# Kernel optimization log

Hardware: AMD Instinct MI355X
Metric: run time of the kernel (lower is better)

## Reference

```python
import jax, jax.numpy as jnp
import numpy as np

EPS = 1.1920929e-07  # torch RMSNorm default eps = finfo(float32).eps

def rmsnorm(x, w):
    return x * jax.lax.rsqrt(jnp.mean(x * x, axis=-1, keepdims=True) + EPS) * w

def setup_inputs() -> dict:
    key = jax.random.key(0)
    ks = jax.random.split(key, 12)
    D, H, SC, ST = 1024, 16, 64, 16
    B, T = 2, 2048
    s = 0.02
    return {
        "x": jax.random.normal(ks[0], (B, T, D), jnp.float32),
        "qkv_w": jax.random.normal(ks[1], (3 * D, D), jnp.float32) * s,
        "o_w": jax.random.normal(ks[2], (D, D), jnp.float32) * s,
        "norm1_w": jnp.ones((D,), jnp.float32),
        "norm2_w": jnp.ones((D,), jnp.float32),
        "in_w": jax.random.normal(ks[3], (SC, D), jnp.float32) * s,
        "out_w": jax.random.normal(ks[4], (D, SC), jnp.float32) * s,  # zeros in torch init; randn for nontrivial baseline
        "A_log": jax.random.normal(ks[5], (SC, ST), jnp.float32) * 0.1,
        "Bp_w": jax.random.normal(ks[6], (ST, SC), jnp.float32) * s,
        "Cp_w": jax.random.normal(ks[7], (ST, SC), jnp.float32) * s,
        "dt_w": jax.random.normal(ks[8], (SC, SC), jnp.float32) * s,
        "dt_b": jnp.full((SC,), -3.0, jnp.float32),
        "gate_w": jax.random.normal(ks[9], (SC, D), jnp.float32) * s,
    }

def selective_scan(h, in_w, out_w, A_log, Bp_w, Cp_w, dt_w, dt_b, gate_w):
    B, T, D = h.shape
    SC, ST = A_log.shape
    z = h @ in_w.T                      # [B,T,SC]
    gate = jax.nn.silu(h @ gate_w.T)    # [B,T,SC]
    A = -jnp.exp(A_log)                 # [SC,ST]
    Bi = z @ Bp_w.T                     # [B,T,ST]
    Ci = z @ Cp_w.T                     # [B,T,ST]
    dt = jax.nn.softplus(z @ dt_w.T + dt_b)  # [B,T,SC]
    A_bar = 1.0 + dt[..., None] * A     # [B,T,SC,ST]

    def step(state, inp):
        a_bar, dtz_t, b_t, c_t = inp    # [B,SC,ST],[B,SC],[B,ST],[B,ST]
        state = a_bar * state + dtz_t[:, :, None] * b_t[:, None, :]
        y = jnp.sum(state * c_t[:, None, :], axis=-1)  # [B,SC]
        return state, y

    init = jnp.zeros((B, SC, ST), h.dtype)
    xs = (jnp.swapaxes(A_bar, 0, 1), jnp.swapaxes(dt * z, 0, 1),
          jnp.swapaxes(Bi, 0, 1), jnp.swapaxes(Ci, 0, 1))
    _, ys = jax.lax.scan(step, init, xs)      # [T,B,SC]
    y = jnp.swapaxes(ys, 0, 1) * gate         # [B,T,SC]
    return y @ out_w.T                        # [B,T,D]

def reference(x, qkv_w, o_w, norm1_w, norm2_w, in_w, out_w, A_log, Bp_w, Cp_w, dt_w, dt_b, gate_w):
    B, T, D = x.shape
    H = 16
    hd = D // H
    h = rmsnorm(x, norm1_w)
    qkv = (h @ qkv_w.T).reshape(B, T, 3, H, hd)
    qkv = jnp.transpose(qkv, (2, 0, 3, 1, 4))  # [3,B,H,T,hd]
    q, k, v = qkv[0], qkv[1], qkv[2]
    attn = jnp.einsum('bhqd,bhkd->bhqk', q, k) / np.sqrt(hd).astype(np.float32)
    mask = jnp.tril(jnp.ones((T, T), bool))
    attn = jnp.where(mask, attn, -jnp.inf)
    attn = jax.nn.softmax(attn, axis=-1)
    out = jnp.einsum('bhqk,bhkd->bhqd', attn, v)
    out = jnp.transpose(out, (0, 2, 1, 3)).reshape(B, T, D)
    x = x + out @ o_w.T
    h2 = rmsnorm(x, norm2_w)
    x = x + selective_scan(h2, in_w, out_w, A_log, Bp_w, Cp_w, dt_w, dt_b, gate_w)
    return x
```

## Files before the change

kernel.cpp:

```cpp
#include <hip/hip_runtime.h>
#include <hip/hip_bf16.h>
#include <math.h>

typedef __hip_bfloat16 bf16;
typedef __attribute__((ext_vector_type(4))) float v_f32x4;
typedef __attribute__((ext_vector_type(4))) unsigned short v_u16x4;
typedef __attribute__((ext_vector_type(8))) unsigned short v_u16x8;
typedef __attribute__((ext_vector_type(8))) __bf16 v_bf16x8;
typedef __attribute__((ext_vector_type(4))) __bf16 v_bf16x4;
typedef __attribute__((ext_vector_type(4))) short v_s16x4;

#define NB 2
#define NT 2048
#define ND 1024
#define NH 16
#define NSC 64
#define NST 16
#define NM (NB*NT)
#define RMS_EPS 1.1920929e-07f
#define NCHUNK 32
#define CLEN 64

__device__ inline float b2f(unsigned short u) {
  union { unsigned int i; float f; } v; v.i = ((unsigned int)u) << 16; return v.f;
}
__device__ inline unsigned short f2b(float f) {
  union { float f; unsigned int i; } v; v.f = f;
  unsigned int r = (v.i + 0x7FFF + ((v.i >> 16) & 1)) >> 16;
  return (unsigned short)r;
}

__device__ inline v_f32x4 mfma16(v_bf16x4 a, v_bf16x4 b, v_f32x4 c) {
#if __has_builtin(__builtin_amdgcn_mfma_f32_16x16x16_bf16)
  return __builtin_amdgcn_mfma_f32_16x16x16_bf16(a, b, c, 0, 0, 0);
#else
  union U { v_bf16x4 h; v_s16x4 s; };
  U ua, ub; ua.h = a; ub.h = b;
  return __builtin_amdgcn_mfma_f32_16x16x16bf16_1k(ua.s, ub.s, c, 0, 0, 0);
#endif
}

__device__ inline void gl_lds16(const bf16* g, bf16* l) {
  __builtin_amdgcn_global_load_lds((__attribute__((address_space(1))) void*)g,
                                   (__attribute__((address_space(3))) void*)l,
                                   16, 0, 0);
}

__global__ __launch_bounds__(256) void cvt_rms_kernel(
    const float* __restrict__ qkv_w, const float* __restrict__ o_w,
    const float* __restrict__ out_w, const float* __restrict__ in_w,
    const float* __restrict__ gate_w, const float* __restrict__ dt_w,
    const float* __restrict__ Bp_w, const float* __restrict__ Cp_w,
    bf16* __restrict__ qkvw_b, bf16* __restrict__ ow_b, bf16* __restrict__ outw_b,
    bf16* __restrict__ W1, bf16* __restrict__ W2,
    const float* __restrict__ x, const float* __restrict__ n1w, bf16* __restrict__ h) {
  const int blk = blockIdx.x, t = threadIdx.x;
  if (blk >= 4295) {
    const int row = blk - 4295;
    v_f32x4 xv = *(const v_f32x4*)(x + (size_t)row * ND + t * 4);
    float s = xv[0]*xv[0] + xv[1]*xv[1] + xv[2]*xv[2] + xv[3]*xv[3];
    #pragma unroll
    for (int off = 32; off; off >>= 1) s += __shfl_xor(s, off, 64);
    __shared__ float red[4];
    __shared__ float scale_s;
    if ((t & 63) == 0) red[t >> 6] = s;
    __syncthreads();
    if (t == 0) scale_s = rsqrtf((red[0] + red[1] + red[2] + red[3]) * (1.0f / ND) + RMS_EPS);
    __syncthreads();
    float sc = scale_s;
    v_f32x4 wv = *(const v_f32x4*)(n1w + t * 4);
    v_u16x4 o;
    o[0] = f2b(xv[0] * sc * wv[0]);
    o[1] = f2b(xv[1] * sc * wv[1]);
    o[2] = f2b(xv[2] * sc * wv[2]);
    o[3] = f2b(xv[3] * sc * wv[3]);
    *(v_u16x4*)((unsigned short*)h + (size_t)row * ND + t * 4) = o;
    return;
  }
  const float* src; bf16* dst; int base;
  if (blk < 3072)      { src = qkv_w;  dst = qkvw_b;      base = blk; }
  else if (blk < 4096) { src = o_w;    dst = ow_b;        base = blk - 3072; }
  else if (blk < 4160) { src = out_w;  dst = outw_b;      base = blk - 4096; }
  else if (blk < 4224) { src = in_w;   dst = W1;          base = blk - 4160; }
  else if (blk < 4288) { src = gate_w; dst = W1 + 65536;  base = blk - 4224; }
  else if (blk < 4292) { src = dt_w;   dst = W2;          base = blk - 4288; }
  else if (blk == 4292){ src = Bp_w;   dst = W2 + 4096;   base = 0; }
  else if (blk == 4293){ src = Cp_w;   dst = W2 + 5120;   base = 0; }
  else {
    v_u16x8 z;
    #pragma unroll
    for (int i = 0; i < 8; i++) z[i] = 0;
    *(v_u16x8*)(W2 + 6144 + t * 8) = z;
    return;
  }
  int i = base * 256 + t;
  v_f32x4 v = ((const v_f32x4*)src)[i];
  v_u16x4 o;
  o[0] = f2b(v[0]); o[1] = f2b(v[1]); o[2] = f2b(v[2]); o[3] = f2b(v[3]);
  ((v_u16x4*)dst)[i] = o;
}

template <bool RES, bool OUTF32>
__global__ __launch_bounds__(256) void gemm_bt_kernel(
    const bf16* __restrict__ A, const bf16* __restrict__ Bw,
    const float* __restrict__ res, void* __restrict__ Cout, int N, int K, int lda) {
  __shared__ alignas(16) bf16 As[128 * 32];
  __shared__ alignas(16) bf16 Bs[128 * 32];
  const int tid = threadIdx.x;
  const int wid = tid >> 6;
  const int lane = tid & 63;
  const int c = lane & 15;
  const int quad = lane >> 4;
  const int m0 = blockIdx.y * 128;
  const int n0 = blockIdx.x * 128;
  const int wm = (wid >> 1) * 64;
  const int wn = (wid & 1) * 64;
  const int srow = tid >> 2;
  const int schunk = tid & 3;

  const bf16* Ap0 = A + (size_t)(m0 + srow) * lda + schunk * 8;
  const bf16* Ap1 = Ap0 + (size_t)64 * lda;
  const bf16* Bp0 = Bw + (size_t)(n0 + srow) * K + schunk * 8;
  const bf16* Bp1 = Bp0 + (size_t)64 * K;
  bf16* AsW0 = As + wid * 512;
  bf16* AsW1 = As + 2048 + wid * 512;
  bf16* BsW0 = Bs + wid * 512;
  bf16* BsW1 = Bs + 2048 + wid * 512;

  v_f32x4 acc[4][4];
  #pragma unroll
  for (int i = 0; i < 4; i++)
    #pragma unroll
    for (int j = 0; j < 4; j++)
      #pragma unroll
      for (int r = 0; r < 4; r++) acc[i][j][r] = 0.0f;

  const int nk = K >> 5;
  for (int kt = 0; kt < nk; kt++) {
    gl_lds16(Ap0 + kt * 32, AsW0);
    gl_lds16(Ap1 + kt * 32, AsW1);
    gl_lds16(Bp0 + kt * 32, BsW0);
    gl_lds16(Bp1 + kt * 32, BsW1);
    __syncthreads();
    v_bf16x8 af[4], bfw[4];
    #pragma unroll
    for (int i = 0; i < 4; i++)
      af[i] = *(const v_bf16x8*)&As[(wm + i * 16 + c) * 32 + quad * 8];
    #pragma unroll
    for (int j = 0; j < 4; j++)
      bfw[j] = *(const v_bf16x8*)&Bs[(wn + j * 16 + c) * 32 + quad * 8];
    #pragma unroll
    for (int i = 0; i < 4; i++)
      #pragma unroll
      for (int j = 0; j < 4; j++)
        acc[i][j] = __builtin_amdgcn_mfma_f32_16x16x32_bf16(af[i], bfw[j], acc[i][j], 0, 0, 0);
    __syncthreads();
  }

  #pragma unroll
  for (int i = 0; i < 4; i++)
    #pragma unroll
    for (int j = 0; j < 4; j++)
      #pragma unroll
      for (int r = 0; r < 4; r++) {
        int rg = m0 + wm + i * 16 + quad * 4 + r;
        int cg = n0 + wn + j * 16 + c;
        size_t idx = (size_t)rg * N + cg;
        float v = acc[i][j][r];
        if (RES) v += res[idx];
        if (OUTF32) ((float*)Cout)[idx] = v;
        else ((bf16*)Cout)[idx] = __float2bfloat16(v);
      }
}

template <bool RES, bool OUTF32>
__global__ __launch_bounds__(256) void gemm_bt64_kernel(
    const bf16* __restrict__ A, const bf16* __restrict__ Bw,
    const float* __restrict__ res, void* __restrict__ Cout, int N, int K, int lda) {
  __shared__ alignas(16) bf16 As[64 * 32];
  __shared__ alignas(16) bf16 Bs[128 * 32];
  const int tid = threadIdx.x;
  const int wid = tid >> 6;
  const int lane = tid & 63;
  const int c = lane & 15;
  const int quad = lane >> 4;
  const int m0 = blockIdx.y * 64;
  const int n0 = blockIdx.x * 128;
  const int wm = (wid & 1) * 32;
  const int wn = (wid >> 1) * 64;
  const int srow = tid >> 2;
  const int schunk = tid & 3;

  const bf16* Ap = A + (size_t)(m0 + srow) * lda + schunk * 8;
  const bf16* Bp0 = Bw + (size_t)(n0 + srow) * K + schunk * 8;
  const bf16* Bp1 = Bp0 + (size_t)64 * K;
  bf16* AsW  = As + wid * 512;
  bf16* BsW0 = Bs + wid * 512;
  bf16* BsW1 = Bs + 2048 + wid * 512;

  v_f32x4 acc[2][4];
  #pragma unroll
  for (int i = 0; i < 2; i++)
    #pragma unroll
    for (int j = 0; j < 4; j++)
      #pragma unroll
      for (int r = 0; r < 4; r++) acc[i][j][r] = 0.0f;

  const int nk = K >> 5;
  for (int kt = 0; kt < nk; kt++) {
    gl_lds16(Ap + kt * 32, AsW);
    gl_lds16(Bp0 + kt * 32, BsW0);
    gl_lds16(Bp1 + kt * 32, BsW1);
    __syncthreads();
    v_bf16x8 af[2], bfw[4];
    #pragma unroll
    for (int i = 0; i < 2; i++)
      af[i] = *(const v_bf16x8*)&As[(wm + i * 16 + c) * 32 + quad * 8];
    #pragma unroll
    for (int j = 0; j < 4; j++)
      bfw[j] = *(const v_bf16x8*)&Bs[(wn + j * 16 + c) * 32 + quad * 8];
    #pragma unroll
    for (int i = 0; i < 2; i++)
      #pragma unroll
      for (int j = 0; j < 4; j++)
        acc[i][j] = __builtin_amdgcn_mfma_f32_16x16x32_bf16(af[i], bfw[j], acc[i][j], 0, 0, 0);
    __syncthreads();
  }

  #pragma unroll
  for (int i = 0; i < 2; i++)
    #pragma unroll
    for (int j = 0; j < 4; j++)
      #pragma unroll
      for (int r = 0; r < 4; r++) {
        int rg = m0 + wm + i * 16 + quad * 4 + r;
        int cg = n0 + wn + j * 16 + c;
        size_t idx = (size_t)rg * N + cg;
        float v = acc[i][j][r];
        if (RES) v += res[idx];
        if (OUTF32) ((float*)Cout)[idx] = v;
        else ((bf16*)Cout)[idx] = __float2bfloat16(v);
      }
}

__global__ __launch_bounds__(256) void vtrans_kernel(const bf16* __restrict__ qkv,
                                                     bf16* __restrict__ VtG) {
  __shared__ alignas(16) bf16 Vs[64 * 72];
  const int tid = threadIdx.x;
  const int t0 = blockIdx.x * 64;
  const int bh = blockIdx.y;
  const int b = bh >> 4, h = bh & 15;
  const int srow = tid >> 2, schunk = tid & 3;
  {
    const bf16* src = qkv + (size_t)(b * NT + t0 + srow) * 3072 + 2048 + h * 64 + schunk * 16;
    *(v_u16x8*)&Vs[srow * 72 + schunk * 16] = *(const v_u16x8*)src;
    *(v_u16x8*)&Vs[srow * 72 + schunk * 16 + 8] = *(const v_u16x8*)(src + 8);
  }
  __syncthreads();
  const unsigned short* Vsu = (const unsigned short*)Vs;
  v_u16x8 a, bvec;
  #pragma unroll
  for (int i = 0; i < 8; i++) a[i] = Vsu[(schunk * 16 + i) * 72 + srow];
  #pragma unroll
  for (int i = 0; i < 8; i++) bvec[i] = Vsu[(schunk * 16 + 8 + i) * 72 + srow];
  bf16* dst = VtG + (size_t)(bh * 64 + srow) * NT + t0 + schunk * 16;
  *(v_u16x8*)dst = a;
  *(v_u16x8*)(dst + 8) = bvec;
}

__global__ __launch_bounds__(256) void attn_kernel(const bf16* __restrict__ qkv,
                                                   const bf16* __restrict__ VtG,
                                                   bf16* __restrict__ out) {
  __shared__ alignas(16) bf16 Qs[64 * 72];
  __shared__ alignas(16) bf16 Ks[64 * 72];
  __shared__ alignas(16) bf16 Vt[64 * 72];
  const int tid = threadIdx.x;
  const int w = tid >> 6;
  const int lane = tid & 63;
  const int c = lane & 15;
  const int quad = lane >> 4;
  const int id = blockIdx.x;
  const int bh = id & 31;
  const int j5 = id >> 5;
  const int j0 = j5 & 7;
  const int qt = (j5 & 24) | (((j5 >> 3) & 1) ? (7 - j0) : j0);
  const int b = bh >> 4;
  const int h = bh & 15;
  const int srow = tid >> 2;
  const int schunk = tid & 3;

  {
    const bf16* src = qkv + (size_t)(b * NT + qt * 64 + srow) * 3072 + h * 64 + schunk * 16;
    *(v_u16x8*)&Qs[srow * 72 + schunk * 16] = *(const v_u16x8*)src;
    *(v_u16x8*)&Qs[srow * 72 + schunk * 16 + 8] = *(const v_u16x8*)(src + 8);
  }
  __syncthreads();
  v_bf16x8 aq0 = *(const v_bf16x8*)&Qs[(w * 16 + c) * 72 + quad * 8];
  v_bf16x8 aq1 = *(const v_bf16x8*)&Qs[(w * 16 + c) * 72 + 32 + quad * 8];

  float l_part = 0.0f;
  v_f32x4 o[4];
  #pragma unroll
  for (int jd = 0; jd < 4; jd++)
    #pragma unroll
    for (int r = 0; r < 4; r++) o[jd][r] = 0.0f;

  const int qrow = w * 16 + c;

  for (int kt = 0; kt <= qt; kt++) {
    {
      const bf16* ksrc = qkv + (size_t)(b * NT + kt * 64 + srow) * 3072 + 1024 + h * 64 + schunk * 16;
      *(v_u16x8*)&Ks[srow * 72 + schunk * 16] = *(const v_u16x8*)ksrc;
      *(v_u16x8*)&Ks[srow * 72 + schunk * 16 + 8] = *(const v_u16x8*)(ksrc + 8);
      const bf16* vsrc = VtG + (size_t)(bh * 64 + srow) * NT + kt * 64 + schunk * 16;
      *(v_u16x8*)&Vt[srow * 72 + schunk * 16] = *(const v_u16x8*)vsrc;
      *(v_u16x8*)&Vt[srow * 72 + schunk * 16 + 8] = *(const v_u16x8*)(vsrc + 8);
    }
    __syncthreads();

    const bool diag = (kt == qt);
    v_bf16x4 pf[4];
    #pragma unroll
    for (int j = 0; j < 4; j++) {
      v_bf16x8 ak0 = *(const v_bf16x8*)&Ks[(j * 16 + c) * 72 + quad * 8];
      v_bf16x8 ak1 = *(const v_bf16x8*)&Ks[(j * 16 + c) * 72 + 32 + quad * 8];
      v_f32x4 z;
      #pragma unroll
      for (int r = 0; r < 4; r++) z[r] = 0.0f;
      z = __builtin_amdgcn_mfma_f32_16x16x32_bf16(ak0, aq0, z, 0, 0, 0);
      z = __builtin_amdgcn_mfma_f32_16x16x32_bf16(ak1, aq1, z, 0, 0, 0);
      v_u16x4 pu;
      #pragma unroll
      for (int r = 0; r < 4; r++) {
        float p = __expf(z[r] * 0.125f);
        if (diag && (j * 16 + quad * 4 + r) > qrow) p = 0.0f;
        l_part += p;
        pu[r] = f2b(p);
      }
      union { v_u16x4 u; v_bf16x4 h; } cv; cv.u = pu;
      pf[j] = cv.h;
    }
    #pragma unroll
    for (int jd = 0; jd < 4; jd++)
      #pragma unroll
      for (int j = 0; j < 4; j++) {
        v_bf16x4 av = *(const v_bf16x4*)&Vt[(jd * 16 + c) * 72 + j * 16 + quad * 4];
        o[jd] = mfma16(av, pf[j], o[jd]);
      }
    __syncthreads();
  }

  float l = l_part;
  l += __shfl_xor(l, 16, 64);
  l += __shfl_xor(l, 32, 64);
  const float inv = 1.0f / l;

  const int qg = qt * 64 + w * 16 + c;
  #pragma unroll
  for (int jd = 0; jd < 4; jd++) {
    v_u16x4 ov;
    #pragma unroll
    for (int r = 0; r < 4; r++) ov[r] = f2b(o[jd][r] * inv);
    *(v_u16x4*)((unsigned short*)out + (size_t)(b * NT + qg) * ND + h * 64 + jd * 16 + quad * 4) = ov;
  }
}

__global__ __launch_bounds__(256) void proj_scan_kernel(
    const float* __restrict__ x1, const float* __restrict__ n2w,
    const bf16* __restrict__ W1, const bf16* __restrict__ W2,
    const float* __restrict__ dt_b,
    float* __restrict__ dt_a, float* __restrict__ dtz_a,
    float* __restrict__ gate_a, float* __restrict__ P2) {
  __shared__ alignas(16) bf16 h2S[16 * 1032];
  __shared__ alignas(16) bf16 Bs[128 * 32];
  __shared__ alignas(16) bf16 zgS[16 * 136];
  const int tid = threadIdx.x;
  const int w = tid >> 6, lane = tid & 63, c = lane & 15, quad = lane >> 4;
  const int m0 = blockIdx.x * 16;
  unsigned short* h2Su = (unsigned short*)h2S;
  unsigned short* zgSu = (unsigned short*)zgS;

  {
    const int r16 = tid >> 4, ct = tid & 15;
    const float* xr = x1 + (size_t)(m0 + r16) * ND + ct * 64;
    v_f32x4 xv[16];
    float ss = 0.0f;
    #pragma unroll
    for (int i = 0; i < 16; i++) {
      xv[i] = *(const v_f32x4*)(xr + i * 4);
      ss += xv[i][0]*xv[i][0] + xv[i][1]*xv[i][1] + xv[i][2]*xv[i][2] + xv[i][3]*xv[i][3];
    }
    ss += __shfl_xor(ss, 1, 64);
    ss += __shfl_xor(ss, 2, 64);
    ss += __shfl_xor(ss, 4, 64);
    ss += __shfl_xor(ss, 8, 64);
    float sc = rsqrtf(ss * (1.0f / ND) + RMS_EPS);
    const float* wr = n2w + ct * 64;
    #pragma unroll
    for (int i = 0; i < 16; i++) {
      v_f32x4 wv = *(const v_f32x4*)(wr + i * 4);
      v_u16x4 o;
      o[0] = f2b(xv[i][0] * sc * wv[0]);
      o[1] = f2b(xv[i][1] * sc * wv[1]);
      o[2] = f2b(xv[i][2] * sc * wv[2]);
      o[3] = f2b(xv[i][3] * sc * wv[3]);
      *(v_u16x4*)&h2Su[r16 * 1032 + ct * 64 + i * 4] = o;
    }
  }
  __syncthreads();

  const int lrow = lane >> 2, lk = lane & 3;
  v_f32x4 acc[2];
  #pragma unroll
  for (int j = 0; j < 2; j++)
    #pragma unroll
    for (int r = 0; r < 4; r++) acc[j][r] = 0.0f;
  for (int kt = 0; kt < 32; kt++) {
    gl_lds16(W1 + (size_t)(w * 32 + lrow) * 1024 + kt * 32 + lk * 8, Bs + (w * 32) * 32);
    gl_lds16(W1 + (size_t)(w * 32 + 16 + lrow) * 1024 + kt * 32 + lk * 8, Bs + (w * 32 + 16) * 32);
    __syncthreads();
    v_bf16x8 af = *(const v_bf16x8*)&h2S[c * 1032 + kt * 32 + quad * 8];
    #pragma unroll
    for (int j = 0; j < 2; j++) {
      v_bf16x8 bfw = *(const v_bf16x8*)&Bs[(w * 32 + j * 16 + c) * 32 + quad * 8];
      acc[j] = __builtin_amdgcn_mfma_f32_16x16x32_bf16(af, bfw, acc[j], 0, 0, 0);
    }
    __syncthreads();
  }
  #pragma unroll
  for (int j = 0; j < 2; j++)
    #pragma unroll
    for (int r = 0; r < 4; r++)
      zgSu[(quad * 4 + r) * 136 + w * 32 + j * 16 + c] = f2b(acc[j][r]);
  __syncthreads();

  v_f32x4 acc2[2];
  #pragma unroll
  for (int j = 0; j < 2; j++)
    #pragma unroll
    for (int r = 0; r < 4; r++) acc2[j][r] = 0.0f;
  for (int kt = 0; kt < 2; kt++) {
    gl_lds16(W2 + (size_t)(w * 32 + lrow) * 64 + kt * 32 + lk * 8, Bs + (w * 32) * 32);
    gl_lds16(W2 + (size_t)(w * 32 + 16 + lrow) * 64 + kt * 32 + lk * 8, Bs + (w * 32 + 16) * 32);
    __syncthreads();
    v_bf16x8 af = *(const v_bf16x8*)&zgS[c * 136 + kt * 32 + quad * 8];
    #pragma unroll
    for (int j = 0; j < 2; j++) {
      v_bf16x8 bfw = *(const v_bf16x8*)&Bs[(w * 32 + j * 16 + c) * 32 + quad * 8];
      acc2[j] = __builtin_amdgcn_mfma_f32_16x16x32_bf16(af, bfw, acc2[j], 0, 0, 0);
    }
    __syncthreads();
  }

  #pragma unroll
  for (int j = 0; j < 2; j++)
    #pragma unroll
    for (int r = 0; r < 4; r++) {
      const int row = quad * 4 + r;
      const int col = w * 32 + j * 16 + c;
      const size_t grow = (size_t)(m0 + row);
      if (w < 2) {
        float z = b2f(zgSu[row * 136 + col]);
        float a = acc2[j][r] + dt_b[col];
        float dt = (a > 20.0f) ? a : log1pf(__expf(a));
        dt_a[grow * NSC + col] = dt;
        dtz_a[grow * NSC + col] = dt * z;
      } else {
        P2[grow * 128 + col] = acc2[j][r];
        float g = b2f(zgSu[row * 136 + col]);
        gate_a[grow * NSC + (col - 64)] = g / (1.0f + __expf(-g));
      }
    }
}

__global__ __launch_bounds__(256) void scanA_kernel(
    const float* __restrict__ dt_a, const float* __restrict__ dtz_a,
    const float* __restrict__ P2, const float* __restrict__ A_log,
    float* __restrict__ Pbuf, float* __restrict__ Sbuf) {
  __shared__ float dtS[CLEN * 16], dtzS[CLEN * 16], biS[CLEN * 16];
  const int k = blockIdx.x, scg = blockIdx.y, b = blockIdx.z;
  const int tid = threadIdx.x;
  const int t0 = k * CLEN;
  {
    int r = tid >> 2, c4 = (tid & 3) * 4;
    *(v_f32x4*)&dtS[r * 16 + c4]  = *(const v_f32x4*)&dt_a[(size_t)(b * NT + t0 + r) * NSC + scg * 16 + c4];
    *(v_f32x4*)&dtzS[r * 16 + c4] = *(const v_f32x4*)&dtz_a[(size_t)(b * NT + t0 + r) * NSC + scg * 16 + c4];
    *(v_f32x4*)&biS[r * 16 + c4]  = *(const v_f32x4*)&P2[(size_t)(b * NT + t0 + r) * 128 + 64 + c4];
  }
  __syncthreads();
  const int st = tid & 15, scl = tid >> 4;
  const float A = -__expf(A_log[(scg * 16 + scl) * NST + st]);
  float P = 1.0f, s = 0.0f;
  #pragma unroll
  for (int t = 0; t < CLEN; t++) {
    float a = fmaf(dtS[t * 16 + scl], A, 1.0f);
    float u = dtzS[t * 16 + scl] * biS[t * 16 + st];
    P *= a;
    s = fmaf(a, s, u);
  }
  size_t idx = (size_t)(b * NCHUNK + k) * 1024 + scg * 256 + tid;
  Pbuf[idx] = P;
  Sbuf[idx] = s;
}

__global__ __launch_bounds__(256) void scanC_kernel(
    const float* __restrict__ dt_a, const float* __restrict__ dtz_a,
    const float* __restrict__ P2, const float* __restrict__ gate_a,
    const float* __restrict__ A_log, const float* __restrict__ Pbuf,
    const float* __restrict__ Sbuf, bf16* __restrict__ ys) {
  __shared__ float dtS[CLEN * 16], dtzS[CLEN * 16], biS[CLEN * 16], ciS[CLEN * 16], gS[CLEN * 16];
  const int k = blockIdx.x, scg = blockIdx.y, b = blockIdx.z;
  const int tid = threadIdx.x;
  const int t0 = k * CLEN;
  {
    int r = tid >> 2, c4 = (tid & 3) * 4;
    *(v_f32x4*)&dtS[r * 16 + c4]  = *(const v_f32x4*)&dt_a[(size_t)(b * NT + t0 + r) * NSC + scg * 16 + c4];
    *(v_f32x4*)&dtzS[r * 16 + c4] = *(const v_f32x4*)&dtz_a[(size_t)(b * NT + t0 + r) * NSC + scg * 16 + c4];
    *(v_f32x4*)&biS[r * 16 + c4]  = *(const v_f32x4*)&P2[(size_t)(b * NT + t0 + r) * 128 + 64 + c4];
    *(v_f32x4*)&ciS[r * 16 + c4]  = *(const v_f32x4*)&P2[(size_t)(b * NT + t0 + r) * 128 + 80 + c4];
    *(v_f32x4*)&gS[r * 16 + c4]   = *(const v_f32x4*)&gate_a[(size_t)(b * NT + t0 + r) * NSC + scg * 16 + c4];
  }
  const int st = tid & 15, scl = tid >> 4;
  const float A = -__expf(A_log[(scg * 16 + scl) * NST + st]);
  float s = 0.0f;
  for (int kk = 0; kk < k; kk++) {
    size_t idx = (size_t)(b * NCHUNK + kk) * 1024 + scg * 256 + tid;
    s = fmaf(Pbuf[idx], s, Sbuf[idx]);
  }
  __syncthreads();
  for (int t = 0; t < CLEN; t++) {
    float a = fmaf(dtS[t * 16 + scl], A, 1.0f);
    float u = dtzS[t * 16 + scl] * biS[t * 16 + st];
    s = fmaf(a, s, u);
    float pv = s * ciS[t * 16 + st];
    pv += __shfl_xor(pv, 1, 64);
    pv += __shfl_xor(pv, 2, 64);
    pv += __shfl_xor(pv, 4, 64);
    pv += __shfl_xor(pv, 8, 64);
    if (st == 0)
      ys[(size_t)(b * NT + t0 + t) * NSC + scg * 16 + scl] = __float2bfloat16(pv * gS[t * 16 + scl]);
  }
}

extern "C" void kernel_launch(void* const* d_in, const int* in_sizes, int n_in,
                              void* d_out, int out_size, void* d_ws, size_t ws_size,
                              hipStream_t stream) {
  const float* x      = (const float*)d_in[0];
  const float* qkv_w  = (const float*)d_in[1];
  const float* o_w    = (const float*)d_in[2];
  const float* n1w    = (const float*)d_in[3];
  const float* n2w    = (const float*)d_in[4];
  const float* in_w   = (const float*)d_in[5];
  const float* out_w  = (const float*)d_in[6];
  const float* A_log  = (const float*)d_in[7];
  const float* Bp_w   = (const float*)d_in[8];
  const float* Cp_w   = (const float*)d_in[9];
  const float* dt_w   = (const float*)d_in[10];
  const float* dt_b   = (const float*)d_in[11];
  const float* gate_w = (const float*)d_in[12];
  float* out = (float*)d_out;

  char* ws = (char*)d_ws;
  size_t off = 0;
  auto alloc = [&](size_t bytes) {
    char* p = ws + off;
    off += (bytes + 255) & ~(size_t)255;
    return p;
  };
  bf16* qkvw_b = (bf16*)alloc((size_t)3 * ND * ND * 2);
  bf16* ow_b   = (bf16*)alloc((size_t)ND * ND * 2);
  bf16* outw_b = (bf16*)alloc((size_t)ND * NSC * 2);
  bf16* W1     = (bf16*)alloc((size_t)128 * ND * 2);
  bf16* W2     = (bf16*)alloc((size_t)128 * NSC * 2);
  char* region0 = alloc((size_t)NM * 3 * ND * 2);
  char* region1 = alloc((size_t)NM * ND * 2);
  bf16* VtG    = (bf16*)alloc((size_t)NB * NH * 64 * NT * 2);
  float* P2    = (float*)alloc((size_t)NM * 128 * 4);
  float* dt_a  = (float*)alloc((size_t)NM * NSC * 4);
  float* dtz_a = (float*)alloc((size_t)NM * NSC * 4);
  float* gate_a= (float*)alloc((size_t)NM * NSC * 4);
  bf16*  ys    = (bf16*)alloc((size_t)NM * NSC * 2);
  float* Pbuf  = (float*)alloc((size_t)NB * NCHUNK * 1024 * 4);
  float* Sbuf  = (float*)alloc((size_t)NB * NCHUNK * 1024 * 4);

  bf16*  qkv     = (bf16*)region0;
  float* x1      = (float*)region0;
  bf16*  h       = (bf16*)region1;
  bf16*  attnout = (bf16*)region1;

  cvt_rms_kernel<<<4295 + NM, 256, 0, stream>>>(qkv_w, o_w, out_w, in_w, gate_w, dt_w,
                                                Bp_w, Cp_w, qkvw_b, ow_b, outw_b, W1, W2,
                                                x, n1w, h);
  gemm_bt_kernel<false, false><<<dim3(3 * ND / 128, NM / 128), 256, 0, stream>>>(
      h, qkvw_b, nullptr, (void*)qkv, 3 * ND, ND, ND);
  vtrans_kernel<<<dim3(NT / 64, NB * NH), 256, 0, stream>>>(qkv, VtG);
  attn_kernel<<<(NT / 64) * NB * NH, 256, 0, stream>>>(qkv, VtG, attnout);
  gemm_bt64_kernel<true, true><<<dim3(ND / 128, NM / 64), 256, 0, stream>>>(
      attnout, ow_b, x, (void*)x1, ND, ND, ND);
  proj_scan_kernel<<<NM / 16, 256, 0, stream>>>(x1, n2w, W1, W2, dt_b,
                                                dt_a, dtz_a, gate_a, P2);
  scanA_kernel<<<dim3(NCHUNK, 4, NB), 256, 0, stream>>>(dt_a, dtz_a, P2, A_log, Pbuf, Sbuf);
  scanC_kernel<<<dim3(NCHUNK, 4, NB), 256, 0, stream>>>(dt_a, dtz_a, P2, gate_a, A_log,
                                                        Pbuf, Sbuf, ys);
  gemm_bt64_kernel<true, true><<<dim3(ND / 128, NM / 64), 256, 0, stream>>>(
      ys, outw_b, x1, (void*)out, ND, NSC, NSC);
}
```

Baseline: 269.8 us.

## Split causal attention KV range across two blocks and fuse V transpose into QKV GEMM

After: 271.8 us. Within noise of the previous version (+0.8%).

```diff
diff --git a/kernel.cpp b/kernel.cpp
--- a/kernel.cpp
+++ b/kernel.cpp
@@ -100,10 +100,11 @@
   ((v_u16x4*)dst)[i] = o;
 }
 
-template <bool RES, bool OUTF32>
+template <bool RES, bool OUTF32, bool VT>
 __global__ __launch_bounds__(256) void gemm_bt_kernel(
     const bf16* __restrict__ A, const bf16* __restrict__ Bw,
-    const float* __restrict__ res, void* __restrict__ Cout, int N, int K, int lda) {
+    const float* __restrict__ res, void* __restrict__ Cout, int N, int K, int lda,
+    bf16* __restrict__ VtG) {
   __shared__ alignas(16) bf16 As[128 * 32];
   __shared__ alignas(16) bf16 Bs[128 * 32];
   const int tid = threadIdx.x;
@@ -155,6 +156,23 @@
       for (int j = 0; j < 4; j++)
         acc[i][j] = __builtin_amdgcn_mfma_f32_16x16x32_bf16(af[i], bfw[j], acc[i][j], 0, 0, 0);
     __syncthreads();
+  }
+
+  if (VT && n0 >= 2048) {
+    #pragma unroll
+    for (int i = 0; i < 4; i++)
+      #pragma unroll
+      for (int j = 0; j < 4; j++) {
+        int hcol = n0 + wn + j * 16 + c - 2048;
+        int hh = hcol >> 6, dd = hcol & 63;
+        int rg0 = m0 + wm + i * 16 + quad * 4;
+        int bb = rg0 >> 11, t0 = rg0 & (NT - 1);
+        v_u16x4 ov;
+        #pragma unroll
+        for (int r = 0; r < 4; r++) ov[r] = f2b(acc[i][j][r]);
+        *(v_u16x4*)((unsigned short*)VtG + ((size_t)((bb * NH + hh) * 64 + dd)) * NT + t0) = ov;
+      }
+    return;
   }
 
   #pragma unroll
@@ -243,34 +261,10 @@
       }
 }
 
-__global__ __launch_bounds__(256) void vtrans_kernel(const bf16* __restrict__ qkv,
-                                                     bf16* __restrict__ VtG) {
-  __shared__ alignas(16) bf16 Vs[64 * 72];
-  const int tid = threadIdx.x;
-  const int t0 = blockIdx.x * 64;
-  const int bh = blockIdx.y;
-  const int b = bh >> 4, h = bh & 15;
-  const int srow = tid >> 2, schunk = tid & 3;
-  {
-    const bf16* src = qkv + (size_t)(b * NT + t0 + srow) * 3072 + 2048 + h * 64 + schunk * 16;
-    *(v_u16x8*)&Vs[srow * 72 + schunk * 16] = *(const v_u16x8*)src;
-    *(v_u16x8*)&Vs[srow * 72 + schunk * 16 + 8] = *(const v_u16x8*)(src + 8);
-  }
-  __syncthreads();
-  const unsigned short* Vsu = (const unsigned short*)Vs;
-  v_u16x8 a, bvec;
-  #pragma unroll
-  for (int i = 0; i < 8; i++) a[i] = Vsu[(schunk * 16 + i) * 72 + srow];
-  #pragma unroll
-  for (int i = 0; i < 8; i++) bvec[i] = Vsu[(schunk * 16 + 8 + i) * 72 + srow];
-  bf16* dst = VtG + (size_t)(bh * 64 + srow) * NT + t0 + schunk * 16;
-  *(v_u16x8*)dst = a;
-  *(v_u16x8*)(dst + 8) = bvec;
-}
-
 __global__ __launch_bounds__(256) void attn_kernel(const bf16* __restrict__ qkv,
                                                    const bf16* __restrict__ VtG,
-                                                   bf16* __restrict__ out) {
+                                                   bf16* __restrict__ OP,
+                                                   float* __restrict__ L) {
   __shared__ alignas(16) bf16 Qs[64 * 72];
   __shared__ alignas(16) bf16 Ks[64 * 72];
   __shared__ alignas(16) bf16 Vt[64 * 72];
@@ -281,13 +275,19 @@
   const int quad = lane >> 4;
   const int id = blockIdx.x;
   const int bh = id & 31;
-  const int j5 = id >> 5;
-  const int j0 = j5 & 7;
-  const int qt = (j5 & 24) | (((j5 >> 3) & 1) ? (7 - j0) : j0);
+  const int u = id >> 5;
+  const int half = u >> 5;
+  const int v = u & 31;
+  const int j0 = v & 7;
+  const int qt = (v & 24) | (((v >> 3) & 1) ? (7 - j0) : j0);
   const int b = bh >> 4;
   const int h = bh & 15;
   const int srow = tid >> 2;
   const int schunk = tid & 3;
+  const int n = qt + 1;
+  const int nh0 = (n + 1) >> 1;
+  const int k0 = half ? nh0 : 0;
+  const int k1 = half ? n : nh0;
 
   {
     const bf16* src = qkv + (size_t)(b * NT + qt * 64 + srow) * 3072 + h * 64 + schunk * 16;
@@ -307,7 +307,7 @@
 
   const int qrow = w * 16 + c;
 
-  for (int kt = 0; kt <= qt; kt++) {
+  for (int kt = k0; kt < k1; kt++) {
     {
       const bf16* ksrc = qkv + (size_t)(b * NT + kt * 64 + srow) * 3072 + 1024 + h * 64 + schunk * 16;
       *(v_u16x8*)&Ks[srow * 72 + schunk * 16] = *(const v_u16x8*)ksrc;
@@ -353,15 +353,39 @@
   float l = l_part;
   l += __shfl_xor(l, 16, 64);
   l += __shfl_xor(l, 32, 64);
-  const float inv = 1.0f / l;
-
-  const int qg = qt * 64 + w * 16 + c;
+
+  const size_t ti = (size_t)((bh * 32 + qt) * 2 + half);
+  if (quad == 0) L[ti * 64 + qrow] = l;
+  unsigned short* OPu = (unsigned short*)OP + (ti * 64 + qrow) * 64;
   #pragma unroll
   for (int jd = 0; jd < 4; jd++) {
     v_u16x4 ov;
     #pragma unroll
-    for (int r = 0; r < 4; r++) ov[r] = f2b(o[jd][r] * inv);
-    *(v_u16x4*)((unsigned short*)out + (size_t)(b * NT + qg) * ND + h * 64 + jd * 16 + quad * 4) = ov;
+    for (int r = 0; r < 4; r++) ov[r] = f2b(o[jd][r]);
+    *(v_u16x4*)(OPu + jd * 16 + quad * 4) = ov;
+  }
+}
+
+__global__ __launch_bounds__(256) void attn_combine_kernel(
+    const bf16* __restrict__ OP, const float* __restrict__ L, bf16* __restrict__ out) {
+  const int bq = blockIdx.x;
+  const int bh = bq >> 5, qt = bq & 31;
+  const int b = bh >> 4, h = bh & 15;
+  const int tid = threadIdx.x;
+  const int q = tid >> 2, dg = (tid & 3) * 16;
+  const size_t ti0 = (size_t)bq * 2;
+  float inv = 1.0f / (L[ti0 * 64 + q] + L[(ti0 + 1) * 64 + q]);
+  const unsigned short* O0 = (const unsigned short*)OP + (ti0 * 64 + q) * 64 + dg;
+  const unsigned short* O1 = (const unsigned short*)OP + ((ti0 + 1) * 64 + q) * 64 + dg;
+  unsigned short* dst = (unsigned short*)out + (size_t)(b * NT + qt * 64 + q) * ND + h * 64 + dg;
+  #pragma unroll
+  for (int i = 0; i < 16; i += 4) {
+    v_u16x4 a = *(const v_u16x4*)(O0 + i);
+    v_u16x4 bb = *(const v_u16x4*)(O1 + i);
+    v_u16x4 o;
+    #pragma unroll
+    for (int r = 0; r < 4; r++) o[r] = f2b((b2f(a[r]) + b2f(bb[r])) * inv);
+    *(v_u16x4*)(dst + i) = o;
   }
 }
 
@@ -582,6 +606,8 @@
   bf16*  ys    = (bf16*)alloc((size_t)NM * NSC * 2);
   float* Pbuf  = (float*)alloc((size_t)NB * NCHUNK * 1024 * 4);
   float* Sbuf  = (float*)alloc((size_t)NB * NCHUNK * 1024 * 4);
+  bf16*  OP    = (bf16*)alloc((size_t)2048 * 64 * 64 * 2);
+  float* Lb    = (float*)alloc((size_t)2048 * 64 * 4);
 
   bf16*  qkv     = (bf16*)region0;
   float* x1      = (float*)region0;
@@ -591,10 +617,10 @@
   cvt_rms_kernel<<<4295 + NM, 256, 0, stream>>>(qkv_w, o_w, out_w, in_w, gate_w, dt_w,
                                                 Bp_w, Cp_w, qkvw_b, ow_b, outw_b, W1, W2,
                                                 x, n1w, h);
-  gemm_bt_kernel<false, false><<<dim3(3 * ND / 128, NM / 128), 256, 0, stream>>>(
-      h, qkvw_b, nullptr, (void*)qkv, 3 * ND, ND, ND);
-  vtrans_kernel<<<dim3(NT / 64, NB * NH), 256, 0, stream>>>(qkv, VtG);
-  attn_kernel<<<(NT / 64) * NB * NH, 256, 0, stream>>>(qkv, VtG, attnout);
+  gemm_bt_kernel<false, false, true><<<dim3(3 * ND / 128, NM / 128), 256, 0, stream>>>(
+      h, qkvw_b, nullptr, (void*)qkv, 3 * ND, ND, ND, VtG);
+  attn_kernel<<<2048, 256, 0, stream>>>(qkv, VtG, OP, Lb);
+  attn_combine_kernel<<<1024, 256, 0, stream>>>(OP, Lb, attnout);
   gemm_bt64_kernel<true, true><<<dim3(ND / 128, NM / 64), 256, 0, stream>>>(
       attnout, ow_b, x, (void*)x1, ND, ND, ND);
   proj_scan_kernel<<<NM / 16, 256, 0, stream>>>(x1, n2w, W1, W2, dt_b,
```
